# Optimization experiments

Measured on AMD Instinct MI355X. Metric: run time of the kernel, lower is better.

## Reference

```python
import jax, jax.numpy as jnp
import numpy as np


def setup_inputs() -> dict:
    key = jax.random.key(0)
    k1, k2 = jax.random.split(key)
    B, H, V, N = 256, 4096, 1024, 32
    v = jax.random.uniform(k1, (B, V, N), dtype=jnp.float32)
    W = jax.random.normal(k2, (H, V, N), dtype=jnp.float32) / np.sqrt(V * N + 2)
    b_h = jnp.zeros((H,), dtype=jnp.float32)
    b_v = jnp.zeros((V, N), dtype=jnp.float32)
    return {"v": v, "W": W, "b_h": b_h, "b_v": b_v}


def reference(v, W, b_h, b_v):
    # (v.unsqueeze(-3) * W).sum([-1,-2]) is a contraction over (visible, category):
    # einsum 'bvn,hvn->bh' — a GEMM with K = n_visible * n.
    logits = jnp.einsum('bvn,hvn->bh', v, W) + b_h          # [B, H]
    sp = jax.nn.softplus(logits).sum(-1)                     # [B]
    vt = jnp.einsum('bvn,vn->b', v, b_v)                     # [B]
    return sp + vt
```

## Files before the change

### kernel.cpp

```cpp
#include <hip/hip_runtime.h>
#include <hip/hip_bf16.h>
#include <stdint.h>

#define B_ 256
#define H_ 4096
#define K_ 32768

typedef __attribute__((ext_vector_type(8))) short bf16x8;
typedef __attribute__((ext_vector_type(4))) float f32x4;

__device__ __forceinline__ unsigned short f2bf(float x) {
    union { float f; unsigned int u; } c; c.f = x;
    unsigned int r = c.u + 0x7FFFu + ((c.u >> 16) & 1u);
    return (unsigned short)(r >> 16);
}

__device__ __forceinline__ short bfc(float x) {
    __hip_bfloat16 h = __float2bfloat16(x);
    union { __hip_bfloat16 h; short s; } c; c.h = h;
    return c.s;
}

__device__ __forceinline__ float softplus_f(float x) {
    return fmaxf(x, 0.0f) + log1pf(expf(-fabsf(x)));
}

__global__ __launch_bounds__(256) void prep_kernel(
    const float* __restrict__ v, const float* __restrict__ bv,
    __hip_bfloat16* __restrict__ vbf, float* __restrict__ vt)
{
    const int b = blockIdx.x;
    const int t = threadIdx.x;
    const float* vr = v + (size_t)b * K_;
    unsigned short* dr = (unsigned short*)(vbf + (size_t)b * K_);
    float acc = 0.f;
    for (int i = t * 8; i < K_; i += 256 * 8) {
        float4 x0 = *(const float4*)(vr + i);
        float4 x1 = *(const float4*)(vr + i + 4);
        float4 b0 = *(const float4*)(bv + i);
        float4 b1 = *(const float4*)(bv + i + 4);
        acc += x0.x*b0.x + x0.y*b0.y + x0.z*b0.z + x0.w*b0.w
             + x1.x*b1.x + x1.y*b1.y + x1.z*b1.z + x1.w*b1.w;
        ushort4 u0, u1;
        u0.x = f2bf(x0.x); u0.y = f2bf(x0.y); u0.z = f2bf(x0.z); u0.w = f2bf(x0.w);
        u1.x = f2bf(x1.x); u1.y = f2bf(x1.y); u1.z = f2bf(x1.z); u1.w = f2bf(x1.w);
        *(ushort4*)(dr + i)     = u0;
        *(ushort4*)(dr + i + 4) = u1;
    }
    __shared__ float sm[256];
    sm[t] = acc;
    __syncthreads();
    for (int s = 128; s > 0; s >>= 1) {
        if (t < s) sm[t] += sm[t + s];
        __syncthreads();
    }
    if (t == 0) vt[b] = sm[0];
}


#define STAGE_W(slot, kt) do {                                                         \
    _Pragma("unroll")                                                                  \
    for (int p_ = 0; p_ < 2; ++p_) {                                                   \
        __builtin_amdgcn_global_load_lds(                                              \
            (const __attribute__((address_space(1))) unsigned int*)(wsrc[p_] + (size_t)(kt) * 64), \
            (__attribute__((address_space(3))) unsigned int*)(&wbuf[(slot)][wldsoff[p_]]), \
            16, 0, 0);                                                                 \
    } } while (0)

#define LOAD_A(dst, kt) do {                                                           \
    _Pragma("unroll")                                                                  \
    for (int m_ = 0; m_ < 2; ++m_)                                                     \
      _Pragma("unroll")                                                                \
      for (int s_ = 0; s_ < 2; ++s_)                                                   \
        dst[m_*2+s_] = *(const bf16x8*)(ap[m_] + (size_t)(kt) * 64 + s_ * 32);         \
    } while (0)

#define COMPUTE(AUSE, T_) do {                                                         \
    const float* wb_ = &wbuf[(T_) & 3][0];                                             \
    _Pragma("unroll")                                                                  \
    for (int s_ = 0; s_ < 2; ++s_) {                                                   \
      bf16x8 bfr[4];                                                                   \
      _Pragma("unroll")                                                                \
      for (int n_ = 0; n_ < 4; ++n_) {                                                 \
        int row_ = n_ * 16 + lr;                                                       \
        int m7_  = row_ & 7;                                                           \
        int g0_  = s_ * 8 + lg * 2;                                                    \
        float4 lo_ = *(const float4*)&wb_[row_ * 64 + (((g0_    ) ^ m7_) << 2)];       \
        float4 hi_ = *(const float4*)&wb_[row_ * 64 + (((g0_ + 1) ^ m7_) << 2)];       \
        bf16x8 t_;                                                                     \
        t_[0]=bfc(lo_.x); t_[1]=bfc(lo_.y); t_[2]=bfc(lo_.z); t_[3]=bfc(lo_.w);        \
        t_[4]=bfc(hi_.x); t_[5]=bfc(hi_.y); t_[6]=bfc(hi_.z); t_[7]=bfc(hi_.w);        \
        bfr[n_] = t_;                                                                  \
      }                                                                                \
      _Pragma("unroll")                                                                \
      for (int m_ = 0; m_ < 2; ++m_)                                                   \
        _Pragma("unroll")                                                              \
        for (int n_ = 0; n_ < 4; ++n_)                                                 \
          acc[m_][n_] = __builtin_amdgcn_mfma_f32_16x16x32_bf16(                       \
              AUSE[m_*2+s_], bfr[n_], acc[m_][n_], 0, 0, 0);                           \
    } } while (0)

#define WAIT_BAR(VMSTR) \
    asm volatile("s_waitcnt " VMSTR "\n\ts_barrier" ::: "memory")

#define BODY(T_, AUSE, ALOAD, ISSW, ISSA, VMSTR) do {                                  \
    if (ISSA) LOAD_A(ALOAD, (T_) + 1);                                                 \
    if (ISSW) STAGE_W(((T_) + 2) & 3, (T_) + 2);                                       \
    WAIT_BAR(VMSTR);                                                                   \
    COMPUTE(AUSE, T_);                                                                 \
    } while (0)

__global__ __launch_bounds__(512, 2) void gemm_kernel(
    const __hip_bfloat16* __restrict__ vbf,
    const float* __restrict__ W,
    float* __restrict__ part,
    int KS, int NT)
{
    __shared__ __align__(16) float wbuf[4][64 * 64];

    const int tid  = threadIdx.x;
    const int wid  = tid >> 6;
    const int lane = tid & 63;
    const int lr   = lane & 15;
    const int lg   = lane >> 4;

    const int bid   = blockIdx.x;
    const int sidx  = bid % KS;
    const int ht    = bid / KS;
    const int h0    = ht * 64;
    const int kbase = sidx * (NT * 64);

    const float* wsrc[2];
    int wldsoff[2];
    #pragma unroll
    for (int p = 0; p < 2; ++p) {
        int f   = p * 512 + tid;
        int row = f >> 4;
        int gl  = f & 15;
        int g   = gl ^ (row & 7);
        wsrc[p]    = W + (size_t)(h0 + row) * K_ + kbase + g * 4;
        wldsoff[p] = (p * 512 + wid * 64) * 4;
    }

    const __hip_bfloat16* ap[2];
    #pragma unroll
    for (int m = 0; m < 2; ++m)
        ap[m] = vbf + (size_t)(wid * 32 + m * 16 + lr) * K_ + kbase + lg * 8;

    f32x4 acc[2][4];
    #pragma unroll
    for (int m = 0; m < 2; ++m)
        #pragma unroll
        for (int n = 0; n < 4; ++n)
            acc[m][n] = (f32x4)(0.0f);

    bf16x8 aA[4], aB[4];

    LOAD_A(aA, 0);
    STAGE_W(0, 0);
    STAGE_W(1, 1);
    asm volatile("" ::: "memory");

    for (int t = 0; t < NT - 2; t += 2) {
        BODY(t,     aA, aB, true, true, "vmcnt(8)");
        BODY(t + 1, aB, aA, true, true, "vmcnt(8)");
    }
    BODY(NT - 2, aA, aB, false, true,  "vmcnt(6)");
    BODY(NT - 1, aB, aA, false, false, "vmcnt(0)");

    float* pout = part + (size_t)sidx * ((size_t)B_ * H_) + h0;
    #pragma unroll
    for (int m = 0; m < 2; ++m)
        #pragma unroll
        for (int n = 0; n < 4; ++n)
            #pragma unroll
            for (int j = 0; j < 4; ++j) {
                int brow = wid * 32 + m * 16 + lg * 4 + j;
                int hcol = n * 16 + lr;
                pout[(size_t)brow * H_ + hcol] = acc[m][n][j];
            }
}

__global__ __launch_bounds__(256) void reduce_kernel(
    const float* __restrict__ part, const float* __restrict__ bh,
    const float* __restrict__ vt, float* __restrict__ out, int KS)
{
    const int b = blockIdx.x;
    const int t = threadIdx.x;
    float sp = 0.f;
    const float* pb = part + (size_t)b * H_;
    for (int h = t * 4; h < H_; h += 256 * 4) {
        float4 l = *(const float4*)(bh + h);
        for (int s = 0; s < KS; ++s) {
            float4 p = *(const float4*)(pb + (size_t)s * B_ * H_ + h);
            l.x += p.x; l.y += p.y; l.z += p.z; l.w += p.w;
        }
        sp += softplus_f(l.x) + softplus_f(l.y) + softplus_f(l.z) + softplus_f(l.w);
    }
    __shared__ float sm[256];
    sm[t] = sp;
    __syncthreads();
    for (int r = 128; r > 0; r >>= 1) {
        if (t < r) sm[t] += sm[t + r];
        __syncthreads();
    }
    if (t == 0) out[b] = sm[0] + vt[b];
}

extern "C" void kernel_launch(void* const* d_in, const int* in_sizes, int n_in,
                              void* d_out, int out_size, void* d_ws, size_t ws_size,
                              hipStream_t stream)
{
    const float* v  = (const float*)d_in[0];
    const float* W  = (const float*)d_in[1];
    const float* bh = (const float*)d_in[2];
    const float* bv = (const float*)d_in[3];
    float* out = (float*)d_out;

    char* ws = (char*)d_ws;
    const size_t vbf_bytes = (size_t)B_ * K_ * sizeof(__hip_bfloat16);
    __hip_bfloat16* vbf = (__hip_bfloat16*)ws;

    int KS = 8;
    while (KS > 1 && vbf_bytes + (size_t)KS * B_ * H_ * 4 + 1024 > ws_size) KS >>= 1;

    float* part = (float*)(ws + vbf_bytes);
    float* vt   = (float*)(ws + vbf_bytes + (size_t)KS * B_ * H_ * 4);

    prep_kernel<<<B_, 256, 0, stream>>>(v, bv, vbf, vt);
    const int NT = (K_ / KS) / 64;
    gemm_kernel<<<(H_ / 64) * KS, 512, 0, stream>>>(vbf, W, part, KS, NT);
    reduce_kernel<<<B_, 256, 0, stream>>>(part, bh, vt, out, KS);
}
```

Baseline: 203.3 us.

## Convert W to bf16 in registers before LDS staging instead of per-read conversion

Replaces direct global-to-LDS fp32 staging of W with register loads that are converted to bf16 once and written to a swizzled bf16 LDS tile. The MFMA B-fragment read becomes a single 16-byte LDS load with no per-read conversion, which halves LDS footprint and removes redundant conversions across waves. The smaller LDS footprint permits raising launch bounds to 4 blocks per CU. The cost is extra VGPRs for in-flight W registers, explicit LDS writes and register pressure from the higher occupancy target.

```diff
diff --git a/kernel.cpp b/kernel.cpp
--- a/kernel.cpp
+++ b/kernel.cpp
@@ -58,14 +58,18 @@
 }
 
 
-#define STAGE_W(slot, kt) do {                                                         \
-    _Pragma("unroll")                                                                  \
-    for (int p_ = 0; p_ < 2; ++p_) {                                                   \
-        __builtin_amdgcn_global_load_lds(                                              \
-            (const __attribute__((address_space(1))) unsigned int*)(wsrc[p_] + (size_t)(kt) * 64), \
-            (__attribute__((address_space(3))) unsigned int*)(&wbuf[(slot)][wldsoff[p_]]), \
-            16, 0, 0);                                                                 \
-    } } while (0)
+#define GLOAD_W(dst, kt) do {                                                          \
+    const float* p_ = wsrcp + (size_t)(kt) * 64;                                       \
+    dst[0] = *(const float4*)p_;                                                       \
+    dst[1] = *(const float4*)(p_ + 4);                                                 \
+    } while (0)
+
+#define CVT_WRITE(WG, slot_) do {                                                      \
+    bf16x8 u_;                                                                         \
+    u_[0]=bfc(WG[0].x); u_[1]=bfc(WG[0].y); u_[2]=bfc(WG[0].z); u_[3]=bfc(WG[0].w);    \
+    u_[4]=bfc(WG[1].x); u_[5]=bfc(WG[1].y); u_[6]=bfc(WG[1].z); u_[7]=bfc(WG[1].w);    \
+    *(bf16x8*)&wtile[(slot_)][wslot_off] = u_;                                         \
+    } while (0)
 
 #define LOAD_A(dst, kt) do {                                                           \
     _Pragma("unroll")                                                                  \
@@ -76,21 +80,15 @@
     } while (0)
 
 #define COMPUTE(AUSE, T_) do {                                                         \
-    const float* wb_ = &wbuf[(T_) & 3][0];                                             \
+    const unsigned short* wb_ = &wtile[(T_) & 3][0];                                   \
     _Pragma("unroll")                                                                  \
     for (int s_ = 0; s_ < 2; ++s_) {                                                   \
       bf16x8 bfr[4];                                                                   \
       _Pragma("unroll")                                                                \
       for (int n_ = 0; n_ < 4; ++n_) {                                                 \
-        int row_ = n_ * 16 + lr;                                                       \
-        int m7_  = row_ & 7;                                                           \
-        int g0_  = s_ * 8 + lg * 2;                                                    \
-        float4 lo_ = *(const float4*)&wb_[row_ * 64 + (((g0_    ) ^ m7_) << 2)];       \
-        float4 hi_ = *(const float4*)&wb_[row_ * 64 + (((g0_ + 1) ^ m7_) << 2)];       \
-        bf16x8 t_;                                                                     \
-        t_[0]=bfc(lo_.x); t_[1]=bfc(lo_.y); t_[2]=bfc(lo_.z); t_[3]=bfc(lo_.w);        \
-        t_[4]=bfc(hi_.x); t_[5]=bfc(hi_.y); t_[6]=bfc(hi_.z); t_[7]=bfc(hi_.w);        \
-        bfr[n_] = t_;                                                                  \
+        int row_  = n_ * 16 + lr;                                                      \
+        int slot_ = s_ * 4 + lg;                                                       \
+        bfr[n_] = *(const bf16x8*)&wb_[row_ * 64 + ((slot_ ^ (row_ & 7)) << 3)];       \
       }                                                                                \
       _Pragma("unroll")                                                                \
       for (int m_ = 0; m_ < 2; ++m_)                                                   \
@@ -100,23 +98,24 @@
               AUSE[m_*2+s_], bfr[n_], acc[m_][n_], 0, 0, 0);                           \
     } } while (0)
 
-#define WAIT_BAR(VMSTR) \
-    asm volatile("s_waitcnt " VMSTR "\n\ts_barrier" ::: "memory")
-
-#define BODY(T_, AUSE, ALOAD, ISSW, ISSA, VMSTR) do {                                  \
+#define BODY(T_, AUSE, ALOAD, WGUSE, WGLOAD, ISSA, ISSW, DOCVT, VMSTR) do {            \
     if (ISSA) LOAD_A(ALOAD, (T_) + 1);                                                 \
-    if (ISSW) STAGE_W(((T_) + 2) & 3, (T_) + 2);                                       \
-    WAIT_BAR(VMSTR);                                                                   \
+    if (ISSW) GLOAD_W(WGLOAD, (T_) + 2);                                               \
+    if (DOCVT) {                                                                       \
+        asm volatile("s_waitcnt " VMSTR ::: "memory");                                 \
+        CVT_WRITE(WGUSE, ((T_) + 1) & 3);                                              \
+    }                                                                                  \
+    asm volatile("s_waitcnt lgkmcnt(0)\n\ts_barrier" ::: "memory");                    \
     COMPUTE(AUSE, T_);                                                                 \
     } while (0)
 
-__global__ __launch_bounds__(512, 2) void gemm_kernel(
+__global__ __launch_bounds__(512, 4) void gemm_kernel(
     const __hip_bfloat16* __restrict__ vbf,
     const float* __restrict__ W,
     float* __restrict__ part,
     int KS, int NT)
 {
-    __shared__ __align__(16) float wbuf[4][64 * 64];
+    __shared__ __align__(16) unsigned short wtile[4][64 * 64];
 
     const int tid  = threadIdx.x;
     const int wid  = tid >> 6;
@@ -130,17 +129,10 @@
     const int h0    = ht * 64;
     const int kbase = sidx * (NT * 64);
 
-    const float* wsrc[2];
-    int wldsoff[2];
-    #pragma unroll
-    for (int p = 0; p < 2; ++p) {
-        int f   = p * 512 + tid;
-        int row = f >> 4;
-        int gl  = f & 15;
-        int g   = gl ^ (row & 7);
-        wsrc[p]    = W + (size_t)(h0 + row) * K_ + kbase + g * 4;
-        wldsoff[p] = (p * 512 + wid * 64) * 4;
-    }
+    const int rw = tid >> 3;
+    const int c8 = tid & 7;
+    const float* wsrcp = W + (size_t)(h0 + rw) * K_ + kbase + c8 * 8;
+    const int wslot_off = rw * 64 + ((c8 ^ (rw & 7)) << 3);
 
     const __hip_bfloat16* ap[2];
     #pragma unroll
@@ -155,18 +147,21 @@
             acc[m][n] = (f32x4)(0.0f);
 
     bf16x8 aA[4], aB[4];
+    float4 wgA[2], wgB[2];
 
     LOAD_A(aA, 0);
-    STAGE_W(0, 0);
-    STAGE_W(1, 1);
+    GLOAD_W(wgA, 0);
+    GLOAD_W(wgB, 1);
+    asm volatile("s_waitcnt vmcnt(2)" ::: "memory");
+    CVT_WRITE(wgA, 0);
     asm volatile("" ::: "memory");
 
     for (int t = 0; t < NT - 2; t += 2) {
-        BODY(t,     aA, aB, true, true, "vmcnt(8)");
-        BODY(t + 1, aB, aA, true, true, "vmcnt(8)");
-    }
-    BODY(NT - 2, aA, aB, false, true,  "vmcnt(6)");
-    BODY(NT - 1, aB, aA, false, false, "vmcnt(0)");
+        BODY(t,     aA, aB, wgB, wgA, true, true, true, "vmcnt(6)");
+        BODY(t + 1, aB, aA, wgA, wgB, true, true, true, "vmcnt(6)");
+    }
+    BODY(NT - 2, aA, aB, wgB, wgA, true,  false, true,  "vmcnt(4)");
+    BODY(NT - 1, aB, aA, wgA, wgB, false, false, false, "vmcnt(0)");
 
     float* pout = part + (size_t)sidx * ((size_t)B_ * H_) + h0;
     #pragma unroll
```

New measurement: 247.4 us. 1.22x slower.

## Warp-specialize GEMM with producer warps converting W to bf16 in LDS

Applied to the files above, without the earlier changes.

Splits each block into 8 consumer warps doing MFMA and 2 producer warps. The producers load fp32 W from global memory into registers, convert it to bf16, and write it into a swizzled LDS tile. The H tile doubles to 128 and the split-K factor rises to 16. This removes the per-consumer repeated fp32-to-bf16 conversion and halves the LDS footprint per element. The risks are that two producer warps may not supply enough bandwidth, the block-wide barriers are fragile, and a larger partial-sum buffer must be reduced.

```diff
diff --git a/kernel.cpp b/kernel.cpp
--- a/kernel.cpp
+++ b/kernel.cpp
@@ -58,65 +58,63 @@
 }
 
 
-#define STAGE_W(slot, kt) do {                                                         \
+#define NCONS 8
+
+#define LOAD_AS(S_, kt) do {                                                           \
+    aC[(S_)]     = *(const bf16x8*)(ap[0] + (size_t)(kt) * 64 + (S_) * 32);            \
+    aC[2 + (S_)] = *(const bf16x8*)(ap[1] + (size_t)(kt) * 64 + (S_) * 32);            \
+    } while (0)
+
+#define COMPUTE_S(T_, S_) do {                                                         \
+    const unsigned short* wb_ = &wtile[(T_) & 3][0];                                   \
     _Pragma("unroll")                                                                  \
-    for (int p_ = 0; p_ < 2; ++p_) {                                                   \
-        __builtin_amdgcn_global_load_lds(                                              \
-            (const __attribute__((address_space(1))) unsigned int*)(wsrc[p_] + (size_t)(kt) * 64), \
-            (__attribute__((address_space(3))) unsigned int*)(&wbuf[(slot)][wldsoff[p_]]), \
-            16, 0, 0);                                                                 \
+    for (int q_ = 0; q_ < 2; ++q_) {                                                   \
+        bf16x8 bfr[4];                                                                 \
+        _Pragma("unroll")                                                              \
+        for (int n_ = 0; n_ < 4; ++n_) {                                               \
+            int row_ = (q_ * 4 + n_) * 16 + lr;                                        \
+            bfr[n_] = *(const bf16x8*)&wb_[row_ * 64 +                                 \
+                        ((((S_) * 4 + lg) ^ (row_ & 7)) << 3)];                        \
+        }                                                                              \
+        _Pragma("unroll")                                                              \
+        for (int m_ = 0; m_ < 2; ++m_)                                                 \
+            _Pragma("unroll")                                                          \
+            for (int n_ = 0; n_ < 4; ++n_)                                             \
+                acc[m_][q_ * 4 + n_] = __builtin_amdgcn_mfma_f32_16x16x32_bf16(        \
+                    aC[m_ * 2 + (S_)], bfr[n_], acc[m_][q_ * 4 + n_], 0, 0, 0);        \
     } } while (0)
 
-#define LOAD_A(dst, kt) do {                                                           \
+#define PISS(dst, HIDX) do {                                                           \
     _Pragma("unroll")                                                                  \
-    for (int m_ = 0; m_ < 2; ++m_)                                                     \
-      _Pragma("unroll")                                                                \
-      for (int s_ = 0; s_ < 2; ++s_)                                                   \
-        dst[m_*2+s_] = *(const bf16x8*)(ap[m_] + (size_t)(kt) * 64 + s_ * 32);         \
-    } while (0)
-
-#define COMPUTE(AUSE, T_) do {                                                         \
-    const float* wb_ = &wbuf[(T_) & 3][0];                                             \
+    for (int j_ = 0; j_ < 4; ++j_) {                                                   \
+        const float* p_ = prow[j_] + (size_t)((HIDX) & 1) * 64 * K_                    \
+                                   + (size_t)((HIDX) >> 1) * 64;                       \
+        dst[2*j_]   = *(const float4*)p_;                                              \
+        dst[2*j_+1] = *(const float4*)(p_ + 4);                                        \
+    } } while (0)
+
+#define PWRITE(src, T_, HALF_) do {                                                    \
     _Pragma("unroll")                                                                  \
-    for (int s_ = 0; s_ < 2; ++s_) {                                                   \
-      bf16x8 bfr[4];                                                                   \
-      _Pragma("unroll")                                                                \
-      for (int n_ = 0; n_ < 4; ++n_) {                                                 \
-        int row_ = n_ * 16 + lr;                                                       \
-        int m7_  = row_ & 7;                                                           \
-        int g0_  = s_ * 8 + lg * 2;                                                    \
-        float4 lo_ = *(const float4*)&wb_[row_ * 64 + (((g0_    ) ^ m7_) << 2)];       \
-        float4 hi_ = *(const float4*)&wb_[row_ * 64 + (((g0_ + 1) ^ m7_) << 2)];       \
-        bf16x8 t_;                                                                     \
-        t_[0]=bfc(lo_.x); t_[1]=bfc(lo_.y); t_[2]=bfc(lo_.z); t_[3]=bfc(lo_.w);        \
-        t_[4]=bfc(hi_.x); t_[5]=bfc(hi_.y); t_[6]=bfc(hi_.z); t_[7]=bfc(hi_.w);        \
-        bfr[n_] = t_;                                                                  \
-      }                                                                                \
-      _Pragma("unroll")                                                                \
-      for (int m_ = 0; m_ < 2; ++m_)                                                   \
-        _Pragma("unroll")                                                              \
-        for (int n_ = 0; n_ < 4; ++n_)                                                 \
-          acc[m_][n_] = __builtin_amdgcn_mfma_f32_16x16x32_bf16(                       \
-              AUSE[m_*2+s_], bfr[n_], acc[m_][n_], 0, 0, 0);                           \
+    for (int j_ = 0; j_ < 4; ++j_) {                                                   \
+        int R_ = (HALF_) * 64 + j_ * 16 + pw * 8 + r8;                                 \
+        float4 a_ = src[2*j_], b_ = src[2*j_+1];                                       \
+        bf16x8 u_;                                                                     \
+        u_[0]=bfc(a_.x); u_[1]=bfc(a_.y); u_[2]=bfc(a_.z); u_[3]=bfc(a_.w);            \
+        u_[4]=bfc(b_.x); u_[5]=bfc(b_.y); u_[6]=bfc(b_.z); u_[7]=bfc(b_.w);            \
+        *(bf16x8*)&wtile[(T_) & 3][R_ * 64 + swz] = u_;                                \
     } } while (0)
 
-#define WAIT_BAR(VMSTR) \
-    asm volatile("s_waitcnt " VMSTR "\n\ts_barrier" ::: "memory")
-
-#define BODY(T_, AUSE, ALOAD, ISSW, ISSA, VMSTR) do {                                  \
-    if (ISSA) LOAD_A(ALOAD, (T_) + 1);                                                 \
-    if (ISSW) STAGE_W(((T_) + 2) & 3, (T_) + 2);                                       \
-    WAIT_BAR(VMSTR);                                                                   \
-    COMPUTE(AUSE, T_);                                                                 \
-    } while (0)
-
-__global__ __launch_bounds__(512, 2) void gemm_kernel(
+#define VMW(N)  asm volatile("s_waitcnt vmcnt(" #N ")" ::: "memory")
+#define PBAR()  asm volatile("s_waitcnt lgkmcnt(0)\n\ts_barrier" ::: "memory")
+#define CBAR()  asm volatile("s_barrier" ::: "memory")
+
+__global__ __launch_bounds__(640, 4) void gemm_kernel(
     const __hip_bfloat16* __restrict__ vbf,
     const float* __restrict__ W,
     float* __restrict__ part,
     int KS, int NT)
 {
-    __shared__ __align__(16) float wbuf[4][64 * 64];
+    __shared__ __align__(16) unsigned short wtile[4][128 * 64];
 
     const int tid  = threadIdx.x;
     const int wid  = tid >> 6;
@@ -127,58 +125,77 @@
     const int bid   = blockIdx.x;
     const int sidx  = bid % KS;
     const int ht    = bid / KS;
-    const int h0    = ht * 64;
+    const int h0    = ht * 128;
     const int kbase = sidx * (NT * 64);
 
-    const float* wsrc[2];
-    int wldsoff[2];
-    #pragma unroll
-    for (int p = 0; p < 2; ++p) {
-        int f   = p * 512 + tid;
-        int row = f >> 4;
-        int gl  = f & 15;
-        int g   = gl ^ (row & 7);
-        wsrc[p]    = W + (size_t)(h0 + row) * K_ + kbase + g * 4;
-        wldsoff[p] = (p * 512 + wid * 64) * 4;
-    }
-
-    const __hip_bfloat16* ap[2];
-    #pragma unroll
-    for (int m = 0; m < 2; ++m)
-        ap[m] = vbf + (size_t)(wid * 32 + m * 16 + lr) * K_ + kbase + lg * 8;
-
-    f32x4 acc[2][4];
-    #pragma unroll
-    for (int m = 0; m < 2; ++m)
-        #pragma unroll
-        for (int n = 0; n < 4; ++n)
-            acc[m][n] = (f32x4)(0.0f);
-
-    bf16x8 aA[4], aB[4];
-
-    LOAD_A(aA, 0);
-    STAGE_W(0, 0);
-    STAGE_W(1, 1);
-    asm volatile("" ::: "memory");
-
-    for (int t = 0; t < NT - 2; t += 2) {
-        BODY(t,     aA, aB, true, true, "vmcnt(8)");
-        BODY(t + 1, aB, aA, true, true, "vmcnt(8)");
-    }
-    BODY(NT - 2, aA, aB, false, true,  "vmcnt(6)");
-    BODY(NT - 1, aB, aA, false, false, "vmcnt(0)");
-
-    float* pout = part + (size_t)sidx * ((size_t)B_ * H_) + h0;
-    #pragma unroll
-    for (int m = 0; m < 2; ++m)
-        #pragma unroll
-        for (int n = 0; n < 4; ++n)
+    if (wid < NCONS) {
+        const __hip_bfloat16* ap[2];
+        #pragma unroll
+        for (int m = 0; m < 2; ++m)
+            ap[m] = vbf + (size_t)(wid * 32 + m * 16 + lr) * K_ + kbase + lg * 8;
+
+        f32x4 acc[2][8];
+        #pragma unroll
+        for (int m = 0; m < 2; ++m)
             #pragma unroll
-            for (int j = 0; j < 4; ++j) {
-                int brow = wid * 32 + m * 16 + lg * 4 + j;
-                int hcol = n * 16 + lr;
-                pout[(size_t)brow * H_ + hcol] = acc[m][n][j];
-            }
+            for (int n = 0; n < 8; ++n)
+                acc[m][n] = (f32x4)(0.0f);
+
+        bf16x8 aC[4];
+        LOAD_AS(0, 0);
+        LOAD_AS(1, 0);
+        CBAR();
+
+        for (int t = 0; t < NT; ++t) {
+            const bool last = (t == NT - 1);
+            COMPUTE_S(t, 0);
+            if (!last) LOAD_AS(0, t + 1);
+            COMPUTE_S(t, 1);
+            if (!last) LOAD_AS(1, t + 1);
+            CBAR();
+        }
+
+        float* pout = part + (size_t)sidx * ((size_t)B_ * H_) + h0;
+        #pragma unroll
+        for (int m = 0; m < 2; ++m)
+            #pragma unroll
+            for (int n = 0; n < 8; ++n)
+                #pragma unroll
+                for (int j = 0; j < 4; ++j) {
+                    int brow = wid * 32 + m * 16 + lg * 4 + j;
+                    int hcol = n * 16 + lr;
+                    pout[(size_t)brow * H_ + hcol] = acc[m][n][j];
+                }
+    } else {
+        const int pw = wid - NCONS;
+        const int l8 = lane & 7;
+        const int r8 = lane >> 3;
+        const float* prow[4];
+        #pragma unroll
+        for (int j = 0; j < 4; ++j)
+            prow[j] = W + (size_t)(h0 + j * 16 + pw * 8 + r8) * K_ + kbase + l8 * 8;
+        const int swz = ((l8 ^ r8) << 3);
+
+        float4 bufA[8], bufB[8];
+
+        PISS(bufA, 0);
+        PISS(bufB, 1);
+        VMW(8);  PWRITE(bufA, 0, 0);  PISS(bufA, 2);
+        VMW(8);  PWRITE(bufB, 0, 1);  PISS(bufB, 3);
+        PBAR();
+
+        for (int t = 0; t < NT - 1; ++t) {
+            const bool lastp = (t == NT - 2);
+            VMW(8);
+            PWRITE(bufA, t + 1, 0);
+            if (!lastp) PISS(bufA, 2 * (t + 2));
+            if (lastp) { VMW(0); } else { VMW(8); }
+            PWRITE(bufB, t + 1, 1);
+            if (!lastp) PISS(bufB, 2 * (t + 2) + 1);
+            PBAR();
+        }
+        PBAR();
+    }
 }
 
 __global__ __launch_bounds__(256) void reduce_kernel(
@@ -221,7 +238,7 @@
     const size_t vbf_bytes = (size_t)B_ * K_ * sizeof(__hip_bfloat16);
     __hip_bfloat16* vbf = (__hip_bfloat16*)ws;
 
-    int KS = 8;
+    int KS = 16;
     while (KS > 1 && vbf_bytes + (size_t)KS * B_ * H_ * 4 + 1024 > ws_size) KS >>= 1;
 
     float* part = (float*)(ws + vbf_bytes);
@@ -229,6 +246,6 @@
 
     prep_kernel<<<B_, 256, 0, stream>>>(v, bv, vbf, vt);
     const int NT = (K_ / KS) / 64;
-    gemm_kernel<<<(H_ / 64) * KS, 512, 0, stream>>>(vbf, W, part, KS, NT);
+    gemm_kernel<<<(H_ / 128) * KS, 640, 0, stream>>>(vbf, W, part, KS, NT);
     reduce_kernel<<<B_, 256, 0, stream>>>(part, bh, vt, out, KS);
 }
```

New measurement: 197.3 us (median of 2 runs). 3.0% less time.
